# Kernel optimization log

Measured on AMD Instinct MI355X. Metric: run time of the kernel, lower is better.

## Reference

```python
import jax, jax.numpy as jnp
import numpy as np

N_NODES = 50000
N_EDGES = 640000
HID = 128
IN_DIM = 3
N_LAYERS = 4


def _silu(x):
    return x * jax.nn.sigmoid(x)


def setup_inputs() -> dict:
    key = jax.random.key(0)
    ks = jax.random.split(key, 20)
    s = 0.05
    inp = {
        'nodes': jax.random.normal(ks[0], (N_NODES, IN_DIM), jnp.float32),
        'edges': jax.random.randint(ks[1], (2, N_EDGES), 0, N_NODES, jnp.int32),
        'edge_attr': jax.random.normal(ks[2], (N_EDGES, 1), jnp.float32),
        # embedding: Linear(input_dim, hidden)
        'emb_w': jax.random.normal(ks[3], (IN_DIM, HID), jnp.float32) * s,
        'emb_b': jnp.zeros((HID,), jnp.float32),
        # per-layer GCL params (stacked over layers)
        # edge_mlp: Linear(2*HID + 1, HID) -> SiLU -> Linear(HID, HID) -> SiLU
        'edge_w1': jax.random.normal(ks[4], (N_LAYERS, 2 * HID + 1, HID), jnp.float32) * s,
        'edge_b1': jnp.zeros((N_LAYERS, HID), jnp.float32),
        'edge_w2': jax.random.normal(ks[5], (N_LAYERS, HID, HID), jnp.float32) * s,
        'edge_b2': jnp.zeros((N_LAYERS, HID), jnp.float32),
        # node_mlp: Linear(2*HID, HID) -> SiLU -> Linear(HID, HID)
        'node_w1': jax.random.normal(ks[6], (N_LAYERS, 2 * HID, HID), jnp.float32) * s,
        'node_b1': jnp.zeros((N_LAYERS, HID), jnp.float32),
        'node_w2': jax.random.normal(ks[7], (N_LAYERS, HID, HID), jnp.float32) * s,
        'node_b2': jnp.zeros((N_LAYERS, HID), jnp.float32),
        # decoder: Linear(HID, HID) -> SiLU -> Linear(HID, 3)
        'dec_w1': jax.random.normal(ks[8], (HID, HID), jnp.float32) * s,
        'dec_b1': jnp.zeros((HID,), jnp.float32),
        'dec_w2': jax.random.normal(ks[9], (HID, 3), jnp.float32) * s,
        'dec_b2': jnp.zeros((3,), jnp.float32),
    }
    return inp


def reference(nodes, edges, edge_attr, emb_w, emb_b,
              edge_w1, edge_b1, edge_w2, edge_b2,
              node_w1, node_b1, node_w2, node_b2,
              dec_w1, dec_b1, dec_w2, dec_b2):
    row, col = edges[0], edges[1]
    n = nodes.shape[0]
    h = nodes @ emb_w + emb_b  # [N, HID]
    for l in range(N_LAYERS):
        # edge model: gather endpoints, MLP on [h_src, h_tgt, edge_attr]
        e_in = jnp.concatenate([h[row], h[col], edge_attr], axis=1)  # [E, 2H+1]
        m = _silu(e_in @ edge_w1[l] + edge_b1[l])
        m = _silu(m @ edge_w2[l] + edge_b2[l])  # [E, HID]
        # node model: scatter-sum messages to source nodes, then MLP
        agg = jax.ops.segment_sum(m, row, num_segments=n)  # [N, HID]
        u = jnp.concatenate([h, agg], axis=1)
        u = _silu(u @ node_w1[l] + node_b1[l])
        h = u @ node_w2[l] + node_b2[l]  # recurrent=False: no residual
    out = _silu(h @ dec_w1 + dec_b1)
    return out @ dec_w2 + dec_b2  # [N, 3]
```

## Files before the change

kernel.cpp:

```cpp
#include <hip/hip_runtime.h>

#define N_NODES 50000
#define N_EDGES 640000
#define HID 128
#define N_LAYERS 4

typedef _Float16 f16x8 __attribute__((ext_vector_type(8)));
typedef float f32x16 __attribute__((ext_vector_type(16)));

__device__ __forceinline__ float silu_f(float x) {
    return x * __builtin_amdgcn_rcpf(1.0f + __expf(-x));
}

__device__ __forceinline__ f32x16 zero16() {
    f32x16 z;
#pragma unroll
    for (int i = 0; i < 16; ++i) z[i] = 0.f;
    return z;
}

__global__ void k_embed(const float* __restrict__ nodes, const float* __restrict__ ew,
                        const float* __restrict__ eb, float* __restrict__ h) {
    int idx = blockIdx.x * 256 + threadIdx.x;
    if (idx >= N_NODES * HID) return;
    int i = idx >> 7, c = idx & 127;
    float n0 = nodes[i * 3 + 0], n1 = nodes[i * 3 + 1], n2 = nodes[i * 3 + 2];
    h[idx] = n0 * ew[c] + n1 * ew[HID + c] + n2 * ew[2 * HID + c] + eb[c];
}

__global__ void k_hist(const int* __restrict__ row, int* __restrict__ deg) {
    int e = blockIdx.x * 256 + threadIdx.x;
    if (e < N_EDGES) atomicAdd(&deg[row[e]], 1);
}

__global__ __launch_bounds__(1024) void k_scan(const int* __restrict__ deg, int* __restrict__ off) {
    __shared__ int partial[1024];
    const int t = threadIdx.x;
    const int chunk = (N_NODES + 1023) / 1024;
    const int base = t * chunk;
    int s = 0;
    for (int i = 0; i < chunk; ++i) {
        int idx = base + i;
        if (idx < N_NODES) s += deg[idx];
    }
    partial[t] = s;
    __syncthreads();
    for (int o = 1; o < 1024; o <<= 1) {
        int v = (t >= o) ? partial[t - o] : 0;
        __syncthreads();
        partial[t] += v;
        __syncthreads();
    }
    int run = (t == 0) ? 0 : partial[t - 1];
    for (int i = 0; i < chunk; ++i) {
        int idx = base + i;
        if (idx < N_NODES) {
            off[idx] = run;
            run += deg[idx];
        }
    }
}

__global__ void k_scatter(const int* __restrict__ row, const int* __restrict__ col,
                          const float* __restrict__ ea, int* __restrict__ off,
                          int* __restrict__ row_s, int* __restrict__ col_s,
                          float* __restrict__ ea_s) {
    int e = blockIdx.x * 256 + threadIdx.x;
    if (e >= N_EDGES) return;
    int r = row[e];
    int pos = atomicAdd(&off[r], 1);
    row_s[pos] = r;
    col_s[pos] = col[e];
    ea_s[pos] = ea[e];
}

__global__ __launch_bounds__(256) void k_packW2(const float* __restrict__ W2all,
                                                _Float16* __restrict__ W2p) {
    const int layer = blockIdx.x;
    const float* W2 = W2all + (size_t)layer * 128 * 128;
    _Float16* out = W2p + (size_t)layer * 128 * 128;
    const int t = threadIdx.x;
    for (int fl = t; fl < 2048; fl += 256) {
        int blk = fl >> 6, lane = fl & 63;
        int cb = blk >> 3, kb = blk & 7;
        int colg = cb * 32 + (lane & 31);
        int kbase = kb * 16 + (lane >> 5) * 8;
        f16x8 v;
#pragma unroll
        for (int j = 0; j < 8; ++j)
            v[j] = (_Float16)W2[(size_t)(kbase + j) * 128 + colg];
        *(f16x8*)&out[(size_t)fl * 8] = v;
    }
}

__global__ __launch_bounds__(256) void k_packAll(
    const float* __restrict__ ew1, const float* __restrict__ nw1,
    const float* __restrict__ nw2, const float* __restrict__ dw1,
    _Float16* __restrict__ WpA, _Float16* __restrict__ WpB,
    _Float16* __restrict__ WpN1, _Float16* __restrict__ WpN2,
    _Float16* __restrict__ WpD1) {
    const int b = blockIdx.x;
    const float* W; _Float16* dst; int K16;
    if (b < 4)       { W = ew1 + (size_t)b * 257 * 128;              dst = WpA  + (size_t)b * 32768; K16 = 8; }
    else if (b < 8)  { int l = b - 4;  W = ew1 + (size_t)l * 257 * 128 + 128 * 128; dst = WpB + (size_t)l * 32768; K16 = 8; }
    else if (b < 12) { int l = b - 8;  W = nw1 + (size_t)l * 256 * 128; dst = WpN1 + (size_t)l * 65536; K16 = 16; }
    else if (b < 16) { int l = b - 12; W = nw2 + (size_t)l * 128 * 128; dst = WpN2 + (size_t)l * 32768; K16 = 8; }
    else             { W = dw1; dst = WpD1; K16 = 8; }
    for (int fl = threadIdx.x; fl < K16 * 256; fl += 256) {
        int lane = fl & 63, cb = (fl >> 6) & 3, ks = fl >> 8;
        int col = cb * 32 + (lane & 31);
        int kb = ks * 16 + (lane >> 5) * 8;
        f16x8 h8, l8;
#pragma unroll
        for (int j = 0; j < 8; ++j) {
            float wv = W[(size_t)(kb + j) * 128 + col];
            _Float16 hh = (_Float16)wv;
            h8[j] = hh;
            l8[j] = (_Float16)((wv - (float)hh) * 2048.0f);
        }
        *(f16x8*)&dst[((size_t)(0 * K16 + ks) * 4 + cb) * 512 + lane * 8] = h8;
        *(f16x8*)&dst[((size_t)(1 * K16 + ks) * 4 + cb) * 512 + lane * 8] = l8;
    }
}

__device__ __forceinline__ void split8(const float* xv, f16x8& xh, f16x8& xl) {
#pragma unroll
    for (int q = 0; q < 8; ++q) {
        _Float16 hh = (_Float16)xv[q];
        xh[q] = hh;
        xl[q] = (_Float16)((xv[q] - (float)hh) * 2048.0f);
    }
}

__global__ __launch_bounds__(512) void k_gemm3(
    const float* __restrict__ X1, const float* __restrict__ X2,
    const _Float16* __restrict__ Wp0, const float* __restrict__ bias0, float* __restrict__ out0,
    const _Float16* __restrict__ Wp1, const float* __restrict__ bias1, float* __restrict__ out1,
    int M, int K16, int do_silu) {
    const int t = threadIdx.x, w = t >> 6, l = t & 63;
    const int lane31 = l & 31, hi = l >> 5;
    const bool dual = (Wp1 != nullptr);
    int rb, cb0, sel;
    if (dual) { rb = w & 1; sel = w >> 2; cb0 = ((w >> 1) & 1) * 2; }
    else      { rb = w & 3; sel = 0;      cb0 = (w >> 2) * 2; }
    const int mtile = dual ? 64 : 128;
    const int m0 = blockIdx.x * mtile;
    const _Float16* Wp = sel ? Wp1 : Wp0;
    const float* bias = sel ? bias1 : bias0;
    float* out = sel ? out1 : out0;

    int rowg = m0 + rb * 32 + lane31;
    if (rowg >= M) rowg = M - 1;
    const int koff = hi * 8;

    f32x16 aH0 = zero16(), aH1 = zero16(), aL0 = zero16(), aL1 = zero16();
    const f16x8* Wv = (const f16x8*)Wp;
#pragma unroll 4
    for (int ks = 0; ks < K16; ++ks) {
        const float* Xp = (X2 != nullptr && ks >= 8) ? X2 : X1;
        const float* px = &Xp[(size_t)rowg * 128 + (ks & 7) * 16 + koff];
        float xv[8];
        *(float4*)&xv[0] = *(const float4*)px;
        *(float4*)&xv[4] = *(const float4*)(px + 4);
        f16x8 xh, xl;
        split8(xv, xh, xl);
        f16x8 bh0 = Wv[((size_t)ks * 4 + cb0) * 64 + l];
        f16x8 bh1 = Wv[((size_t)ks * 4 + cb0 + 1) * 64 + l];
        f16x8 bl0 = Wv[((size_t)(K16 + ks) * 4 + cb0) * 64 + l];
        f16x8 bl1 = Wv[((size_t)(K16 + ks) * 4 + cb0 + 1) * 64 + l];
        aH0 = __builtin_amdgcn_mfma_f32_32x32x16_f16(xh, bh0, aH0, 0, 0, 0);
        aH1 = __builtin_amdgcn_mfma_f32_32x32x16_f16(xh, bh1, aH1, 0, 0, 0);
        aL0 = __builtin_amdgcn_mfma_f32_32x32x16_f16(xh, bl0, aL0, 0, 0, 0);
        aL0 = __builtin_amdgcn_mfma_f32_32x32x16_f16(xl, bh0, aL0, 0, 0, 0);
        aL1 = __builtin_amdgcn_mfma_f32_32x32x16_f16(xh, bl1, aL1, 0, 0, 0);
        aL1 = __builtin_amdgcn_mfma_f32_32x32x16_f16(xl, bh1, aL1, 0, 0, 0);
    }
    const float inv = 1.0f / 2048.0f;
#pragma unroll
    for (int c = 0; c < 2; ++c) {
        int col = (cb0 + c) * 32 + lane31;
        float bv = bias ? bias[col] : 0.f;
        const f32x16& aH = c ? aH1 : aH0;
        const f32x16& aL = c ? aL1 : aL0;
#pragma unroll
        for (int r = 0; r < 16; ++r) {
            int gr = m0 + rb * 32 + (r & 3) + 8 * (r >> 2) + 4 * hi;
            if (gr < M) {
                float v = aH[r] + aL[r] * inv + bv;
                out[(size_t)gr * 128 + col] = do_silu ? silu_f(v) : v;
            }
        }
    }
}

__global__ __launch_bounds__(512, 4) void k_node(
    float* __restrict__ h, const float* __restrict__ agg,
    const _Float16* __restrict__ Wn1, const float* __restrict__ nb1,
    const _Float16* __restrict__ Wn2, const float* __restrict__ nb2,
    const _Float16* __restrict__ WA, const float* __restrict__ ebA,
    const _Float16* __restrict__ WB,
    float* __restrict__ outA, float* __restrict__ outB,
    const _Float16* __restrict__ WD, const float* __restrict__ db1,
    const float* __restrict__ dw2, const float* __restrict__ db2,
    float* __restrict__ dec_out, int M, int final_mode) {
    __shared__ float u_lds[128 * 133];
    __shared__ float w2l[384];
    const int t = threadIdx.x, w = t >> 6, l = t & 63;
    const int lane31 = l & 31, hi = l >> 5;
    const int rb = w & 3, cb0 = (w >> 2) * 2;
    const int m0 = blockIdx.x * 128;
    const int koff = hi * 8;
    const float inv = 1.0f / 2048.0f;

    if (final_mode && t < 384) w2l[t] = dw2[t];

    int rowg = m0 + rb * 32 + lane31;
    if (rowg >= M) rowg = M - 1;

    {
        f32x16 aH0 = zero16(), aH1 = zero16(), aL0 = zero16(), aL1 = zero16();
        const f16x8* Wv = (const f16x8*)Wn1;
#pragma unroll 4
        for (int ks = 0; ks < 16; ++ks) {
            const float* Xp = (ks >= 8) ? agg : h;
            const float* px = &Xp[(size_t)rowg * 128 + (ks & 7) * 16 + koff];
            float xv[8];
            *(float4*)&xv[0] = *(const float4*)px;
            *(float4*)&xv[4] = *(const float4*)(px + 4);
            f16x8 xh, xl;
            split8(xv, xh, xl);
            f16x8 bh0 = Wv[((size_t)ks * 4 + cb0) * 64 + l];
            f16x8 bh1 = Wv[((size_t)ks * 4 + cb0 + 1) * 64 + l];
            f16x8 bl0 = Wv[((size_t)(16 + ks) * 4 + cb0) * 64 + l];
            f16x8 bl1 = Wv[((size_t)(16 + ks) * 4 + cb0 + 1) * 64 + l];
            aH0 = __builtin_amdgcn_mfma_f32_32x32x16_f16(xh, bh0, aH0, 0, 0, 0);
            aH1 = __builtin_amdgcn_mfma_f32_32x32x16_f16(xh, bh1, aH1, 0, 0, 0);
            aL0 = __builtin_amdgcn_mfma_f32_32x32x16_f16(xh, bl0, aL0, 0, 0, 0);
            aL0 = __builtin_amdgcn_mfma_f32_32x32x16_f16(xl, bh0, aL0, 0, 0, 0);
            aL1 = __builtin_amdgcn_mfma_f32_32x32x16_f16(xh, bl1, aL1, 0, 0, 0);
            aL1 = __builtin_amdgcn_mfma_f32_32x32x16_f16(xl, bh1, aL1, 0, 0, 0);
        }
#pragma unroll
        for (int c = 0; c < 2; ++c) {
            int col = (cb0 + c) * 32 + lane31;
            float bv = nb1[col];
            const f32x16& aH = c ? aH1 : aH0;
            const f32x16& aL = c ? aL1 : aL0;
#pragma unroll
            for (int r = 0; r < 16; ++r) {
                int lr = rb * 32 + (r & 3) + 8 * (r >> 2) + 4 * hi;
                u_lds[lr * 133 + col] = silu_f(aH[r] + aL[r] * inv + bv);
            }
        }
    }
    __syncthreads();

    {
        f32x16 aH0 = zero16(), aH1 = zero16(), aL0 = zero16(), aL1 = zero16();
        const f16x8* Wv = (const f16x8*)Wn2;
#pragma unroll
        for (int ks = 0; ks < 8; ++ks) {
            float xv[8];
            const int base = (rb * 32 + lane31) * 133 + ks * 16 + koff;
#pragma unroll
            for (int q = 0; q < 8; ++q) xv[q] = u_lds[base + q];
            f16x8 xh, xl;
            split8(xv, xh, xl);
            f16x8 bh0 = Wv[((size_t)ks * 4 + cb0) * 64 + l];
            f16x8 bh1 = Wv[((size_t)ks * 4 + cb0 + 1) * 64 + l];
            f16x8 bl0 = Wv[((size_t)(8 + ks) * 4 + cb0) * 64 + l];
            f16x8 bl1 = Wv[((size_t)(8 + ks) * 4 + cb0 + 1) * 64 + l];
            aH0 = __builtin_amdgcn_mfma_f32_32x32x16_f16(xh, bh0, aH0, 0, 0, 0);
            aH1 = __builtin_amdgcn_mfma_f32_32x32x16_f16(xh, bh1, aH1, 0, 0, 0);
            aL0 = __builtin_amdgcn_mfma_f32_32x32x16_f16(xh, bl0, aL0, 0, 0, 0);
            aL0 = __builtin_amdgcn_mfma_f32_32x32x16_f16(xl, bh0, aL0, 0, 0, 0);
            aL1 = __builtin_amdgcn_mfma_f32_32x32x16_f16(xh, bl1, aL1, 0, 0, 0);
            aL1 = __builtin_amdgcn_mfma_f32_32x32x16_f16(xl, bh1, aL1, 0, 0, 0);
        }
        __syncthreads();
#pragma unroll
        for (int c = 0; c < 2; ++c) {
            int col = (cb0 + c) * 32 + lane31;
            float bv = nb2[col];
            const f32x16& aH = c ? aH1 : aH0;
            const f32x16& aL = c ? aL1 : aL0;
#pragma unroll
            for (int r = 0; r < 16; ++r) {
                int lr = rb * 32 + (r & 3) + 8 * (r >> 2) + 4 * hi;
                float v = aH[r] + aL[r] * inv + bv;
                u_lds[lr * 133 + col] = v;
                int gr = m0 + lr;
                if (!final_mode && gr < M) h[(size_t)gr * 128 + col] = v;
            }
        }
    }
    __syncthreads();

    if (!final_mode) {
#pragma unroll
        for (int pass = 0; pass < 2; ++pass) {
            const int sel = w >> 2, w2 = w & 3;
            const int cbp = w2 >> 1, cb0p = (cbp) * 2;
            const int rb3 = (w2 & 1) * 2 + pass;
            const _Float16* Wp = sel ? WB : WA;
            float* op = sel ? outB : outA;
            f32x16 aH0 = zero16(), aH1 = zero16(), aL0 = zero16(), aL1 = zero16();
            const f16x8* Wv = (const f16x8*)Wp;
#pragma unroll
            for (int ks = 0; ks < 8; ++ks) {
                float xv[8];
                const int base = (rb3 * 32 + lane31) * 133 + ks * 16 + koff;
#pragma unroll
                for (int q = 0; q < 8; ++q) xv[q] = u_lds[base + q];
                f16x8 xh, xl;
                split8(xv, xh, xl);
                f16x8 bh0 = Wv[((size_t)ks * 4 + cb0p) * 64 + l];
                f16x8 bh1 = Wv[((size_t)ks * 4 + cb0p + 1) * 64 + l];
                f16x8 bl0 = Wv[((size_t)(8 + ks) * 4 + cb0p) * 64 + l];
                f16x8 bl1 = Wv[((size_t)(8 + ks) * 4 + cb0p + 1) * 64 + l];
                aH0 = __builtin_amdgcn_mfma_f32_32x32x16_f16(xh, bh0, aH0, 0, 0, 0);
                aH1 = __builtin_amdgcn_mfma_f32_32x32x16_f16(xh, bh1, aH1, 0, 0, 0);
                aL0 = __builtin_amdgcn_mfma_f32_32x32x16_f16(xh, bl0, aL0, 0, 0, 0);
                aL0 = __builtin_amdgcn_mfma_f32_32x32x16_f16(xl, bh0, aL0, 0, 0, 0);
                aL1 = __builtin_amdgcn_mfma_f32_32x32x16_f16(xh, bl1, aL1, 0, 0, 0);
                aL1 = __builtin_amdgcn_mfma_f32_32x32x16_f16(xl, bh1, aL1, 0, 0, 0);
            }
#pragma unroll
            for (int c = 0; c < 2; ++c) {
                int col = (cb0p + c) * 32 + lane31;
                float bv = sel ? 0.f : ebA[col];
                const f32x16& aH = c ? aH1 : aH0;
                const f32x16& aL = c ? aL1 : aL0;
#pragma unroll
                for (int r = 0; r < 16; ++r) {
                    int gr = m0 + rb3 * 32 + (r & 3) + 8 * (r >> 2) + 4 * hi;
                    if (gr < M) op[(size_t)gr * 128 + col] = aH[r] + aL[r] * inv + bv;
                }
            }
        }
    } else {
        f32x16 aH0 = zero16(), aH1 = zero16(), aL0 = zero16(), aL1 = zero16();
        const f16x8* Wv = (const f16x8*)WD;
#pragma unroll
        for (int ks = 0; ks < 8; ++ks) {
            float xv[8];
            const int base = (rb * 32 + lane31) * 133 + ks * 16 + koff;
#pragma unroll
            for (int q = 0; q < 8; ++q) xv[q] = u_lds[base + q];
            f16x8 xh, xl;
            split8(xv, xh, xl);
            f16x8 bh0 = Wv[((size_t)ks * 4 + cb0) * 64 + l];
            f16x8 bh1 = Wv[((size_t)ks * 4 + cb0 + 1) * 64 + l];
            f16x8 bl0 = Wv[((size_t)(8 + ks) * 4 + cb0) * 64 + l];
            f16x8 bl1 = Wv[((size_t)(8 + ks) * 4 + cb0 + 1) * 64 + l];
            aH0 = __builtin_amdgcn_mfma_f32_32x32x16_f16(xh, bh0, aH0, 0, 0, 0);
            aH1 = __builtin_amdgcn_mfma_f32_32x32x16_f16(xh, bh1, aH1, 0, 0, 0);
            aL0 = __builtin_amdgcn_mfma_f32_32x32x16_f16(xh, bl0, aL0, 0, 0, 0);
            aL0 = __builtin_amdgcn_mfma_f32_32x32x16_f16(xl, bh0, aL0, 0, 0, 0);
            aL1 = __builtin_amdgcn_mfma_f32_32x32x16_f16(xh, bl1, aL1, 0, 0, 0);
            aL1 = __builtin_amdgcn_mfma_f32_32x32x16_f16(xl, bh1, aL1, 0, 0, 0);
        }
        __syncthreads();
#pragma unroll
        for (int c = 0; c < 2; ++c) {
            int col = (cb0 + c) * 32 + lane31;
            float bv = db1[col];
            const f32x16& aH = c ? aH1 : aH0;
            const f32x16& aL = c ? aL1 : aL0;
#pragma unroll
            for (int r = 0; r < 16; ++r) {
                int lr = rb * 32 + (r & 3) + 8 * (r >> 2) + 4 * hi;
                u_lds[lr * 133 + col] = silu_f(aH[r] + aL[r] * inv + bv);
            }
        }
        __syncthreads();
        if (t < 384) {
            int rowl = t & 127, j = t >> 7;
            int gm = m0 + rowl;
            if (gm < M) {
                float s = db2[j];
                for (int c = 0; c < 128; ++c)
                    s += u_lds[rowl * 133 + c] * w2l[c * 3 + j];
                dec_out[(size_t)gm * 3 + j] = s;
            }
        }
    }
}

#define EPI(ACC, CB) { _Pragma("unroll") \
    for (int rr = 0; rr < 16; ++rr) ACC[rr] = silu_f(ACC[rr] + b2v[CB]); }

#define SEGSUM(ACC, CB) { \
    float p = 0.f; \
    _Pragma("unroll") \
    for (int rr = 0; rr < 16; ++rr) { \
        int erow = (rr & 3) + 8 * (rr >> 2) + 4 * hi; \
        p += (erow >= st && erow < en) ? ACC[rr] : 0.f; \
    } \
    p += __shfl_xor(p, 32); \
    if (hi == 0) atomicAdd(&agg[(size_t)rseg * 128 + CB * 32 + lane31], p); }

__global__ __launch_bounds__(256) void k_edge7(
    const float* __restrict__ A, const float* __restrict__ Bm,
    const float* __restrict__ w1last, const float* __restrict__ b2,
    const _Float16* __restrict__ W2p, const int* __restrict__ row_s,
    const int* __restrict__ col_s, const float* __restrict__ ea_s,
    float* __restrict__ agg) {
    __shared__ __align__(16) _Float16 W2s[16384];
    const int t = threadIdx.x;
    for (int i = t; i < 2048; i += 256)
        ((float4*)W2s)[i] = ((const float4*)W2p)[i];
    __syncthreads();

    const int l = t & 63, wv = t >> 6;
    const int lane31 = l & 31, hi = l >> 5;
    const int koff = hi * 8;

    float b2v[4];
#pragma unroll
    for (int cb = 0; cb < 4; ++cb) b2v[cb] = b2[cb * 32 + lane31];

    const f16x8* w2v = (const f16x8*)W2s;
    const int n_wt = N_EDGES / 32;
    const int nw = gridDim.x * 4;

    for (int wt = blockIdx.x * 4 + wv; wt < n_wt; wt += nw) {
        const int e = wt * 32 + lane31;
        const int r = row_s[e];
        const float eav = ea_s[e];
        const float* Ap = A + (size_t)r * 128 + koff;
        const float* Bp = Bm + (size_t)col_s[e] * 128 + koff;

        f32x16 acc0 = zero16(), acc1 = zero16(), acc2 = zero16(), acc3 = zero16();
#pragma unroll
        for (int kb = 0; kb < 8; ++kb) {
            float av[8], bv[8], wl[8];
            *(float4*)&av[0] = *(const float4*)&Ap[kb * 16];
            *(float4*)&av[4] = *(const float4*)&Ap[kb * 16 + 4];
            *(float4*)&bv[0] = *(const float4*)&Bp[kb * 16];
            *(float4*)&bv[4] = *(const float4*)&Bp[kb * 16 + 4];
            *(float4*)&wl[0] = *(const float4*)&w1last[kb * 16 + koff];
            *(float4*)&wl[4] = *(const float4*)&w1last[kb * 16 + koff + 4];
            f16x8 o;
#pragma unroll
            for (int q = 0; q < 8; ++q)
                o[q] = (_Float16)silu_f(av[q] + bv[q] + eav * wl[q]);
            acc0 = __builtin_amdgcn_mfma_f32_32x32x16_f16(o, w2v[(0 * 8 + kb) * 64 + l], acc0, 0, 0, 0);
            acc1 = __builtin_amdgcn_mfma_f32_32x32x16_f16(o, w2v[(1 * 8 + kb) * 64 + l], acc1, 0, 0, 0);
            acc2 = __builtin_amdgcn_mfma_f32_32x32x16_f16(o, w2v[(2 * 8 + kb) * 64 + l], acc2, 0, 0, 0);
            acc3 = __builtin_amdgcn_mfma_f32_32x32x16_f16(o, w2v[(3 * 8 + kb) * 64 + l], acc3, 0, 0, 0);
        }
        EPI(acc0, 0) EPI(acc1, 1) EPI(acc2, 2) EPI(acc3, 3)

        int prev = __shfl_up(r, 1, 32);
        bool flag = (lane31 == 0) || (r != prev);
        unsigned long long bal = __ballot(flag);
        unsigned mask = (unsigned)bal;
        int ns = __popc(mask);
        unsigned mrem = mask;
        for (int s = 0; s < ns; ++s) {
            int st = __ffs(mrem) - 1;
            unsigned mnext = mrem & (mrem - 1);
            int en = mnext ? (__ffs(mnext) - 1) : 32;
            mrem = mnext;
            int rseg = __shfl(r, st, 32);
            SEGSUM(acc0, 0) SEGSUM(acc1, 1) SEGSUM(acc2, 2) SEGSUM(acc3, 3)
        }
    }
}

extern "C" void kernel_launch(void* const* d_in, const int* in_sizes, int n_in,
                              void* d_out, int out_size, void* d_ws, size_t ws_size,
                              hipStream_t stream) {
    const float* nodes = (const float*)d_in[0];
    const int* edges = (const int*)d_in[1];
    const float* ea = (const float*)d_in[2];
    const float* emb_w = (const float*)d_in[3];
    const float* emb_b = (const float*)d_in[4];
    const float* ew1 = (const float*)d_in[5];
    const float* eb1 = (const float*)d_in[6];
    const float* ew2 = (const float*)d_in[7];
    const float* eb2 = (const float*)d_in[8];
    const float* nw1 = (const float*)d_in[9];
    const float* nb1 = (const float*)d_in[10];
    const float* nw2 = (const float*)d_in[11];
    const float* nb2 = (const float*)d_in[12];
    const float* dw1 = (const float*)d_in[13];
    const float* db1 = (const float*)d_in[14];
    const float* dw2 = (const float*)d_in[15];
    const float* db2 = (const float*)d_in[16];
    const int* row = edges;
    const int* col = edges + N_EDGES;

    const size_t NH = (size_t)N_NODES * HID;
    float* r0 = (float*)d_ws;
    float* r1 = r0 + NH;
    float* r2 = r1 + NH;
    float* r3 = r2 + NH;
    int* deg = (int*)(r3 + NH);
    int* off = deg + N_NODES;
    int* row_s = off + N_NODES;
    int* col_s = row_s + N_EDGES;
    float* ea_s = (float*)(col_s + N_EDGES);
    _Float16* W2p = (_Float16*)(ea_s + N_EDGES);
    _Float16* WpA  = W2p  + (size_t)4 * 16384;
    _Float16* WpB  = WpA  + (size_t)4 * 32768;
    _Float16* WpN1 = WpB  + (size_t)4 * 32768;
    _Float16* WpN2 = WpN1 + (size_t)4 * 65536;
    _Float16* WpD1 = WpN2 + (size_t)4 * 32768;

    hipMemsetAsync(deg, 0, N_NODES * sizeof(int), stream);
    k_hist<<<(N_EDGES + 255) / 256, 256, 0, stream>>>(row, deg);
    k_scan<<<1, 1024, 0, stream>>>(deg, off);
    k_scatter<<<(N_EDGES + 255) / 256, 256, 0, stream>>>(row, col, ea, off, row_s, col_s, ea_s);
    k_packW2<<<N_LAYERS, 256, 0, stream>>>(ew2, W2p);
    k_packAll<<<17, 256, 0, stream>>>(ew1, nw1, nw2, dw1, WpA, WpB, WpN1, WpN2, WpD1);

    k_embed<<<(N_NODES * HID + 255) / 256, 256, 0, stream>>>(nodes, emb_w, emb_b, r0);

    const int g64 = (N_NODES + 63) / 64;
    const int g128 = (N_NODES + 127) / 128;

    k_gemm3<<<g64, 512, 0, stream>>>(r0, nullptr,
                                     WpA, eb1, r1,
                                     WpB, nullptr, r2,
                                     N_NODES, 8, 0);

    for (int l = 0; l < N_LAYERS; ++l) {
        hipMemsetAsync(r3, 0, NH * sizeof(float), stream);
        k_edge7<<<1024, 256, 0, stream>>>(r1, r2,
                                          ew1 + (size_t)l * 257 * 128 + 256 * 128,
                                          eb2 + l * 128,
                                          W2p + (size_t)l * 16384,
                                          row_s, col_s, ea_s, r3);
        if (l < N_LAYERS - 1) {
            k_node<<<g128, 512, 0, stream>>>(r0, r3,
                                             WpN1 + (size_t)l * 65536, nb1 + l * 128,
                                             WpN2 + (size_t)l * 32768, nb2 + l * 128,
                                             WpA + (size_t)(l + 1) * 32768, eb1 + (l + 1) * 128,
                                             WpB + (size_t)(l + 1) * 32768,
                                             r1, r2,
                                             nullptr, nullptr, nullptr, nullptr, nullptr,
                                             N_NODES, 0);
        } else {
            k_node<<<g128, 512, 0, stream>>>(r0, r3,
                                             WpN1 + (size_t)l * 65536, nb1 + l * 128,
                                             WpN2 + (size_t)l * 32768, nb2 + l * 128,
                                             nullptr, nullptr, nullptr,
                                             nullptr, nullptr,
                                             WpD1, db1, dw2, db2,
                                             (float*)d_out, N_NODES, 1);
        }
    }
}
```

Baseline: 1.095 ms.

## Split edge-kernel output columns across wave pairs to raise occupancy

Each 32-edge group is now handled by two waves, each computing half of the 128 output columns (two MFMA accumulators instead of four). This halves accumulator register pressure and permits 4 blocks per SM via launch bounds, with the grid doubled to 2048 blocks. The cost is that both waves redundantly gather the A/B endpoint rows and recompute the SiLU input activations, and segment detection runs twice.

Result: slower. 1.444 ms (+31.8%).

```diff
diff --git a/kernel.cpp b/kernel.cpp
--- a/kernel.cpp
+++ b/kernel.cpp
@@ -398,9 +398,9 @@
         p += (erow >= st && erow < en) ? ACC[rr] : 0.f; \
     } \
     p += __shfl_xor(p, 32); \
-    if (hi == 0) atomicAdd(&agg[(size_t)rseg * 128 + CB * 32 + lane31], p); }
-
-__global__ __launch_bounds__(256) void k_edge7(
+    if (hi == 0) atomicAdd(&agg[(size_t)rseg * 128 + (CB) * 32 + lane31], p); }
+
+__global__ __launch_bounds__(256, 4) void k_edge8(
     const float* __restrict__ A, const float* __restrict__ Bm,
     const float* __restrict__ w1last, const float* __restrict__ b2,
     const _Float16* __restrict__ W2p, const int* __restrict__ row_s,
@@ -415,23 +415,24 @@
     const int l = t & 63, wv = t >> 6;
     const int lane31 = l & 31, hi = l >> 5;
     const int koff = hi * 8;
+    const int cbA = (wv & 1) * 2, cbB = cbA + 1;
 
     float b2v[4];
-#pragma unroll
-    for (int cb = 0; cb < 4; ++cb) b2v[cb] = b2[cb * 32 + lane31];
+    b2v[cbA] = b2[cbA * 32 + lane31];
+    b2v[cbB] = b2[cbB * 32 + lane31];
 
     const f16x8* w2v = (const f16x8*)W2s;
-    const int n_wt = N_EDGES / 32;
-    const int nw = gridDim.x * 4;
-
-    for (int wt = blockIdx.x * 4 + wv; wt < n_wt; wt += nw) {
-        const int e = wt * 32 + lane31;
+    const int n_gr = N_EDGES / 32;
+    const int stride = gridDim.x * 2;
+
+    for (int g = blockIdx.x * 2 + (wv >> 1); g < n_gr; g += stride) {
+        const int e = g * 32 + lane31;
         const int r = row_s[e];
         const float eav = ea_s[e];
         const float* Ap = A + (size_t)r * 128 + koff;
         const float* Bp = Bm + (size_t)col_s[e] * 128 + koff;
 
-        f32x16 acc0 = zero16(), acc1 = zero16(), acc2 = zero16(), acc3 = zero16();
+        f32x16 acc0 = zero16(), acc1 = zero16();
 #pragma unroll
         for (int kb = 0; kb < 8; ++kb) {
             float av[8], bv[8], wl[8];
@@ -445,12 +446,10 @@
 #pragma unroll
             for (int q = 0; q < 8; ++q)
                 o[q] = (_Float16)silu_f(av[q] + bv[q] + eav * wl[q]);
-            acc0 = __builtin_amdgcn_mfma_f32_32x32x16_f16(o, w2v[(0 * 8 + kb) * 64 + l], acc0, 0, 0, 0);
-            acc1 = __builtin_amdgcn_mfma_f32_32x32x16_f16(o, w2v[(1 * 8 + kb) * 64 + l], acc1, 0, 0, 0);
-            acc2 = __builtin_amdgcn_mfma_f32_32x32x16_f16(o, w2v[(2 * 8 + kb) * 64 + l], acc2, 0, 0, 0);
-            acc3 = __builtin_amdgcn_mfma_f32_32x32x16_f16(o, w2v[(3 * 8 + kb) * 64 + l], acc3, 0, 0, 0);
-        }
-        EPI(acc0, 0) EPI(acc1, 1) EPI(acc2, 2) EPI(acc3, 3)
+            acc0 = __builtin_amdgcn_mfma_f32_32x32x16_f16(o, w2v[(cbA * 8 + kb) * 64 + l], acc0, 0, 0, 0);
+            acc1 = __builtin_amdgcn_mfma_f32_32x32x16_f16(o, w2v[(cbB * 8 + kb) * 64 + l], acc1, 0, 0, 0);
+        }
+        EPI(acc0, cbA) EPI(acc1, cbB)
 
         int prev = __shfl_up(r, 1, 32);
         bool flag = (lane31 == 0) || (r != prev);
@@ -464,7 +463,7 @@
             int en = mnext ? (__ffs(mnext) - 1) : 32;
             mrem = mnext;
             int rseg = __shfl(r, st, 32);
-            SEGSUM(acc0, 0) SEGSUM(acc1, 1) SEGSUM(acc2, 2) SEGSUM(acc3, 3)
+            SEGSUM(acc0, cbA) SEGSUM(acc1, cbB)
         }
     }
 }
@@ -528,7 +527,7 @@
 
     for (int l = 0; l < N_LAYERS; ++l) {
         hipMemsetAsync(r3, 0, NH * sizeof(float), stream);
-        k_edge7<<<1024, 256, 0, stream>>>(r1, r2,
+        k_edge8<<<2048, 256, 0, stream>>>(r1, r2,
                                           ew1 + (size_t)l * 257 * 128 + 256 * 128,
                                           eb2 + l * 128,
                                           W2p + (size_t)l * 16384,
```
